# Kernel tuning notes

Hardware: AMD Instinct MI355X
Metric: run time of the kernel (lower is better)

## Reference

```python
import jax, jax.numpy as jnp
import numpy as np

H = 256      # hidden_size
NH = 4       # num_heads
HD = H // NH # head_dim
N_NODES = 2048
N_EDGES = 8192
EPS = 1e-5


def _layer_norm(x, g, b):
    mu = jnp.mean(x, axis=-1, keepdims=True)
    var = jnp.mean((x - mu) ** 2, axis=-1, keepdims=True)
    return (x - mu) * jax.lax.rsqrt(var + EPS) * g + b


def setup_inputs() -> dict:
    key = jax.random.key(0)
    ks = jax.random.split(key, 16)
    s = 1.0 / np.sqrt(H)
    inp = {
        "node_features": jax.random.normal(ks[0], (N_NODES, H), jnp.float32),
        "edge_features": jax.random.normal(ks[1], (N_EDGES, H), jnp.float32),
        "in_proj_w": jax.random.uniform(ks[2], (3 * H, H), jnp.float32, -s, s),
        "in_proj_b": jnp.zeros((3 * H,), jnp.float32),
        "out_proj_w": jax.random.uniform(ks[3], (H, H), jnp.float32, -s, s),
        "out_proj_b": jnp.zeros((H,), jnp.float32),
        "mlp_w1": jax.random.uniform(ks[4], (H, H), jnp.float32, -s, s),
        "mlp_b1": jnp.zeros((H,), jnp.float32),
        "mlp_w2": jax.random.uniform(ks[5], (H, H), jnp.float32, -s, s),
        "mlp_b2": jnp.zeros((H,), jnp.float32),
        "nu_w": jax.random.uniform(ks[6], (H, H), jnp.float32, -s, s),
        "nu_b": jnp.zeros((H,), jnp.float32),
        "ln1_g": jnp.ones((H,), jnp.float32),
        "ln1_b": jnp.zeros((H,), jnp.float32),
        "ln2_g": jnp.ones((H,), jnp.float32),
        "ln2_b": jnp.zeros((H,), jnp.float32),
        "edge_index": jax.random.randint(ks[7], (2, N_EDGES), 0, N_NODES, jnp.int32),
    }
    return inp


def reference(node_features, edge_features, in_proj_w, in_proj_b, out_proj_w, out_proj_b,
              mlp_w1, mlp_b1, mlp_w2, mlp_b2, nu_w, nu_b,
              ln1_g, ln1_b, ln2_g, ln2_b, edge_index):
    x = edge_features  # [E, H]; torch MHA with batch=1, seq=E
    qkv = x @ in_proj_w.T + in_proj_b            # [E, 3H]
    q, k, v = jnp.split(qkv, 3, axis=-1)
    q = q.reshape(N_EDGES, NH, HD)
    k = k.reshape(N_EDGES, NH, HD)
    v = v.reshape(N_EDGES, NH, HD)
    scores = jnp.einsum('qhd,khd->hqk', q, k) / np.sqrt(HD)  # [NH, E, E]
    attn = jax.nn.softmax(scores, axis=-1)
    ctx = jnp.einsum('hqk,khd->qhd', attn, v).reshape(N_EDGES, H)
    attended = ctx @ out_proj_w.T + out_proj_b

    e = _layer_norm(edge_features + attended, ln1_g, ln1_b)
    mlp = jax.nn.relu(e @ mlp_w1.T + mlp_b1) @ mlp_w2.T + mlp_b2
    e = _layer_norm(e + mlp, ln2_g, ln2_b)

    dst = edge_index[1]
    seg_sum = jax.ops.segment_sum(e, dst, num_segments=N_NODES)           # [N, H]
    cnt = jax.ops.segment_sum(jnp.ones((N_EDGES,), e.dtype), dst, num_segments=N_NODES)
    node_updates = seg_sum / jnp.maximum(cnt, 1.0)[:, None]               # scatter_mean
    n = node_features + jax.nn.relu(node_updates @ nu_w.T + nu_b)
    return (n, e)
```

## Files before the change

kernel.cpp:

```cpp
#include <hip/hip_runtime.h>

typedef __bf16 bf16_t;
typedef __bf16 bf16x8 __attribute__((ext_vector_type(8)));
typedef __bf16 bf16x4 __attribute__((ext_vector_type(4)));
typedef unsigned short u16x8 __attribute__((ext_vector_type(8)));
typedef unsigned int u32x4 __attribute__((ext_vector_type(4)));
typedef float f32x4 __attribute__((ext_vector_type(4)));
typedef float f32x16 __attribute__((ext_vector_type(16)));
typedef int i32x2 __attribute__((ext_vector_type(2)));

#define NE 8192
#define NN 2048
#define HH 256
#define NSPLIT 8
#define QSCALE 0.18033688011112042f

#if __has_builtin(__builtin_amdgcn_exp2f)
#define EXP2(x) __builtin_amdgcn_exp2f(x)
#else
#define EXP2(x) exp2f(x)
#endif

__device__ inline f32x4 mfma16(bf16x8 a, bf16x8 b, f32x4 c) {
    return __builtin_amdgcn_mfma_f32_16x16x32_bf16(a, b, c, 0, 0, 0);
}
__device__ inline f32x16 mfma32(bf16x8 a, bf16x8 b, f32x16 c) {
    return __builtin_amdgcn_mfma_f32_32x32x16_bf16(a, b, c, 0, 0, 0);
}
__device__ inline unsigned cvtpk(float lo, float hi) {
    unsigned r;
    asm("v_cvt_pk_bf16_f32 %0, %1, %2" : "=v"(r) : "v"(lo), "v"(hi));
    return r;
}
__device__ inline bf16x8 cvt8(float4 a, float4 b) {
    bf16x8 o;
    o[0] = (bf16_t)a.x; o[1] = (bf16_t)a.y; o[2] = (bf16_t)a.z; o[3] = (bf16_t)a.w;
    o[4] = (bf16_t)b.x; o[5] = (bf16_t)b.y; o[6] = (bf16_t)b.z; o[7] = (bf16_t)b.w;
    return o;
}
__device__ inline bf16x4 cvt4(float4 v) {
    bf16x4 o;
    o[0] = (bf16_t)v.x; o[1] = (bf16_t)v.y; o[2] = (bf16_t)v.z; o[3] = (bf16_t)v.w;
    return o;
}

__global__ __launch_bounds__(256)
void convert_kernel(const float* __restrict__ ef, const float* __restrict__ wq,
                    const float* __restrict__ wo, const float* __restrict__ w1,
                    const float* __restrict__ w2, const float* __restrict__ wn,
                    bf16_t* __restrict__ ebf, bf16_t* __restrict__ bwq,
                    bf16_t* __restrict__ bwo, bf16_t* __restrict__ bw1,
                    bf16_t* __restrict__ bw2, bf16_t* __restrict__ bwn) {
    int i = blockIdx.x * 256 + threadIdx.x;
    ((bf16x4*)ebf)[i] = cvt4(((const float4*)ef)[i]);
    if (i < 49152) ((bf16x4*)bwq)[i] = cvt4(((const float4*)wq)[i]);
    if (i < 16384) {
        ((bf16x4*)bwo)[i] = cvt4(((const float4*)wo)[i]);
        ((bf16x4*)bw1)[i] = cvt4(((const float4*)w1)[i]);
        ((bf16x4*)bw2)[i] = cvt4(((const float4*)w2)[i]);
        ((bf16x4*)bwn)[i] = cvt4(((const float4*)wn)[i]);
    }
}

template<int ACT, int OUTKIND, int QSC, int ADIV>
__global__ __launch_bounds__(256)
void gemm_kernel(const void* __restrict__ Av, const bf16_t* __restrict__ B,
                 const float* __restrict__ bias, void* __restrict__ out,
                 const float* __restrict__ resid, const float* __restrict__ cntp,
                 int M, int N, int K) {
    __shared__ bf16_t As[64][72];
    __shared__ bf16_t Bs[64][72];
    int tid = threadIdx.x;
    int w = tid >> 6, l = tid & 63, hi = l >> 4, c15 = l & 15;
    int wr = w >> 1, wc = w & 1;
    int brow = blockIdx.x * 64, bcol = blockIdx.y * 64;
    int r = tid >> 2, s = tid & 3;

    f32x4 acc[2][2] = {};

    for (int k0 = 0; k0 < K; k0 += 64) {
        __syncthreads();
        if (ADIV) {
            const float* Af = (const float*)Av;
            const float* p = &Af[(long)(brow + r) * K + k0 + s * 16];
            float4 f0 = *(const float4*)p,       f1 = *(const float4*)(p + 4);
            float4 f2 = *(const float4*)(p + 8), f3 = *(const float4*)(p + 12);
            float rc = 1.0f / fmaxf(cntp[brow + r], 1.0f);
            f0.x *= rc; f0.y *= rc; f0.z *= rc; f0.w *= rc;
            f1.x *= rc; f1.y *= rc; f1.z *= rc; f1.w *= rc;
            f2.x *= rc; f2.y *= rc; f2.z *= rc; f2.w *= rc;
            f3.x *= rc; f3.y *= rc; f3.z *= rc; f3.w *= rc;
            *(bf16x8*)&As[r][s * 16]     = cvt8(f0, f1);
            *(bf16x8*)&As[r][s * 16 + 8] = cvt8(f2, f3);
        } else {
            const bf16_t* Ab = (const bf16_t*)Av;
            *(bf16x8*)&As[r][s * 16]     = *(const bf16x8*)&Ab[(long)(brow + r) * K + k0 + s * 16];
            *(bf16x8*)&As[r][s * 16 + 8] = *(const bf16x8*)&Ab[(long)(brow + r) * K + k0 + s * 16 + 8];
        }
        *(bf16x8*)&Bs[r][s * 16]     = *(const bf16x8*)&B[(long)(bcol + r) * K + k0 + s * 16];
        *(bf16x8*)&Bs[r][s * 16 + 8] = *(const bf16x8*)&B[(long)(bcol + r) * K + k0 + s * 16 + 8];
        __syncthreads();
#pragma unroll
        for (int c = 0; c < 2; ++c) {
            bf16x8 af0 = *(const bf16x8*)&As[wr * 32 + c15][c * 32 + hi * 8];
            bf16x8 af1 = *(const bf16x8*)&As[wr * 32 + 16 + c15][c * 32 + hi * 8];
            bf16x8 bf0 = *(const bf16x8*)&Bs[wc * 32 + c15][c * 32 + hi * 8];
            bf16x8 bf1 = *(const bf16x8*)&Bs[wc * 32 + 16 + c15][c * 32 + hi * 8];
            acc[0][0] = mfma16(af0, bf0, acc[0][0]);
            acc[0][1] = mfma16(af0, bf1, acc[0][1]);
            acc[1][0] = mfma16(af1, bf0, acc[1][0]);
            acc[1][1] = mfma16(af1, bf1, acc[1][1]);
        }
    }

    float sc = (QSC && bcol < 256) ? QSCALE : 1.0f;
#pragma unroll
    for (int i = 0; i < 2; ++i)
#pragma unroll
        for (int j = 0; j < 2; ++j)
#pragma unroll
            for (int rg = 0; rg < 4; ++rg) {
                int row = brow + wr * 32 + i * 16 + hi * 4 + rg;
                int col = bcol + wc * 32 + j * 16 + c15;
                float v = (acc[i][j][rg] + bias[col]) * sc;
                if (ACT) v = fmaxf(v, 0.0f);
                if (OUTKIND == 0) {
                    ((float*)out)[(long)row * N + col] = v;
                } else if (OUTKIND == 1) {
                    ((bf16_t*)out)[(long)row * N + col] = (bf16_t)v;
                } else {
                    ((float*)out)[(long)row * N + col] =
                        resid[(long)row * N + col] + fmaxf(v, 0.0f);
                }
            }
}

__global__ __launch_bounds__(256, 2)
void attn_kernel(const bf16_t* __restrict__ qkv, bf16_t* __restrict__ Opart,
                 float* __restrict__ lpart) {
    __shared__ char smem[36864];
    bf16_t (*Ks)[64][72] = (bf16_t (*)[64][72])smem;
    bf16_t (*Vt)[64][72] = (bf16_t (*)[64][72])(smem + 18432);

    int h = blockIdx.x & 3, qb = blockIdx.x >> 2, sp = blockIdx.y;
    int q0 = qb * 256;
    int tid = threadIdx.x;
    int wv = tid >> 6, l = tid & 63, l31 = l & 31, h8 = l >> 5;

    bf16x8 qf[2][4];
#pragma unroll
    for (int qt = 0; qt < 2; ++qt)
#pragma unroll
        for (int dc = 0; dc < 4; ++dc)
            qf[qt][dc] = *(const bf16x8*)&qkv[
                (size_t)(q0 + wv * 64 + qt * 32 + l31) * 768 + h * 64 + dc * 16 + h8 * 8];

    f32x16 o[2][2];
#pragma unroll
    for (int a = 0; a < 2; ++a)
#pragma unroll
        for (int b = 0; b < 2; ++b)
#pragma unroll
            for (int r = 0; r < 16; ++r) o[a][b][r] = 0.f;
    float ls[2] = {0.f, 0.f};

    int kr = tid >> 2, ksc = tid & 3;
    int vp = tid & 31, vc = tid >> 5;
    int kv0 = sp * (NE / NSPLIT);
    const int NT = (NE / NSPLIT) / 64;

    bf16x8 kst0, kst1, vst0, vst1;
    {
        const bf16_t* ksrc = &qkv[(size_t)(kv0 + kr) * 768 + 256 + h * 64 + ksc * 16];
        kst0 = *(const bf16x8*)ksrc; kst1 = *(const bf16x8*)(ksrc + 8);
        const bf16_t* vsrc = &qkv[(size_t)(kv0 + 2 * vp) * 768 + 512 + h * 64 + vc * 8];
        vst0 = *(const bf16x8*)vsrc; vst1 = *(const bf16x8*)(vsrc + 768);
    }
    {
        *(bf16x8*)&Ks[0][kr][ksc * 16]     = kst0;
        *(bf16x8*)&Ks[0][kr][ksc * 16 + 8] = kst1;
        u16x8 ua = __builtin_bit_cast(u16x8, vst0), ub = __builtin_bit_cast(u16x8, vst1);
#pragma unroll
        for (int j = 0; j < 8; ++j) {
            unsigned wd = (unsigned)ua[j] | ((unsigned)ub[j] << 16);
            *(unsigned*)&Vt[0][vc * 8 + j][2 * vp] = wd;
        }
    }

    for (int t = 0; t < NT; ++t) {
        int cur = t & 1;
        __syncthreads();
        if (t + 1 < NT) {
            int kt = kv0 + (t + 1) * 64;
            const bf16_t* ksrc = &qkv[(size_t)(kt + kr) * 768 + 256 + h * 64 + ksc * 16];
            kst0 = *(const bf16x8*)ksrc; kst1 = *(const bf16x8*)(ksrc + 8);
            const bf16_t* vsrc = &qkv[(size_t)(kt + 2 * vp) * 768 + 512 + h * 64 + vc * 8];
            vst0 = *(const bf16x8*)vsrc; vst1 = *(const bf16x8*)(vsrc + 768);
        }

#pragma unroll
        for (int kvt = 0; kvt < 2; ++kvt) {
            bf16x8 kf[4];
#pragma unroll
            for (int dc = 0; dc < 4; ++dc)
                kf[dc] = *(const bf16x8*)&Ks[cur][kvt * 32 + l31][dc * 16 + h8 * 8];
            f32x16 s[2];
#pragma unroll
            for (int qt = 0; qt < 2; ++qt) {
#pragma unroll
                for (int r = 0; r < 16; ++r) s[qt][r] = 0.f;
#pragma unroll
                for (int dc = 0; dc < 4; ++dc)
                    s[qt] = mfma32(kf[dc], qf[qt][dc], s[qt]);
            }
            bf16x8 bfr[2][2];
#pragma unroll
            for (int qt = 0; qt < 2; ++qt) {
                float p[16];
#pragma unroll
                for (int r = 0; r < 16; ++r) { p[r] = EXP2(s[qt][r]); ls[qt] += p[r]; }
#pragma unroll
                for (int half = 0; half < 2; ++half) {
                    i32x2 r0 = __builtin_amdgcn_permlane32_swap(
                        (int)cvtpk(p[8 * half + 0], p[8 * half + 1]),
                        (int)cvtpk(p[8 * half + 4], p[8 * half + 5]), false, false);
                    i32x2 r1 = __builtin_amdgcn_permlane32_swap(
                        (int)cvtpk(p[8 * half + 2], p[8 * half + 3]),
                        (int)cvtpk(p[8 * half + 6], p[8 * half + 7]), false, false);
                    u32x4 wds;
                    wds[0] = (unsigned)r0[0]; wds[1] = (unsigned)r1[0];
                    wds[2] = (unsigned)r0[1]; wds[3] = (unsigned)r1[1];
                    bfr[qt][half] = __builtin_bit_cast(bf16x8, wds);
                }
            }
#pragma unroll
            for (int dt = 0; dt < 2; ++dt) {
                bf16x8 vf[2];
#pragma unroll
                for (int half = 0; half < 2; ++half)
                    vf[half] = *(const bf16x8*)&Vt[cur][dt * 32 + l31][(kvt * 2 + half) * 16 + h8 * 8];
#pragma unroll
                for (int qt = 0; qt < 2; ++qt)
#pragma unroll
                    for (int half = 0; half < 2; ++half)
                        o[dt][qt] = mfma32(vf[half], bfr[qt][half], o[dt][qt]);
            }
        }

        if (t + 1 < NT) {
            int nb = (t + 1) & 1;
            *(bf16x8*)&Ks[nb][kr][ksc * 16]     = kst0;
            *(bf16x8*)&Ks[nb][kr][ksc * 16 + 8] = kst1;
            u16x8 ua = __builtin_bit_cast(u16x8, vst0), ub = __builtin_bit_cast(u16x8, vst1);
#pragma unroll
            for (int j = 0; j < 8; ++j) {
                unsigned wd = (unsigned)ua[j] | ((unsigned)ub[j] << 16);
                *(unsigned*)&Vt[nb][vc * 8 + j][2 * vp] = wd;
            }
        }
    }

#pragma unroll
    for (int qt = 0; qt < 2; ++qt) {
        float lt = ls[qt] + __shfl_xor(ls[qt], 32);
        if (l < 32)
            lpart[((size_t)sp * 4 + h) * NE + q0 + wv * 64 + qt * 32 + l31] = lt;
    }

    float* Of = (float*)smem;
#pragma unroll
    for (int pass = 0; pass < 2; ++pass) {
        __syncthreads();
        if ((wv >> 1) == pass) {
#pragma unroll
            for (int dt = 0; dt < 2; ++dt)
#pragma unroll
                for (int qt = 0; qt < 2; ++qt)
#pragma unroll
                    for (int r = 0; r < 16; ++r) {
                        int qrel = (wv & 1) * 64 + qt * 32 + l31;
                        int d = dt * 32 + (r & 3) + 8 * (r >> 2) + 4 * h8;
                        Of[qrel * 68 + d] = o[dt][qt][r];
                    }
        }
        __syncthreads();
        {
            int rr = tid >> 1, hf = tid & 1;
            bf16_t* dst = &Opart[(size_t)sp * NE * 256 +
                                 (size_t)(q0 + pass * 128 + rr) * 256 + h * 64 + hf * 32];
#pragma unroll
            for (int i = 0; i < 4; ++i) {
                float4 va = *(float4*)&Of[rr * 68 + hf * 32 + i * 8];
                float4 vb = *(float4*)&Of[rr * 68 + hf * 32 + i * 8 + 4];
                bf16x8 ob;
                ob[0] = (bf16_t)va.x; ob[1] = (bf16_t)va.y;
                ob[2] = (bf16_t)va.z; ob[3] = (bf16_t)va.w;
                ob[4] = (bf16_t)vb.x; ob[5] = (bf16_t)vb.y;
                ob[6] = (bf16_t)vb.z; ob[7] = (bf16_t)vb.w;
                *(bf16x8*)&dst[i * 8] = ob;
            }
        }
    }
}

__global__ __launch_bounds__(256)
void attn_merge_kernel(const bf16_t* __restrict__ Opart, const float* __restrict__ lpart,
                       bf16_t* __restrict__ ctx) {
    int i = blockIdx.x * 256 + threadIdx.x;
    int q = i >> 5;
    int h = (i & 31) >> 3;
    float sum[8] = {};
    float lsum = 0.f;
#pragma unroll
    for (int sp = 0; sp < NSPLIT; ++sp) {
        bf16x8 v = ((const bf16x8*)Opart)[(size_t)sp * (NE * 32) + i];
#pragma unroll
        for (int j = 0; j < 8; ++j) sum[j] += (float)v[j];
        lsum += lpart[((size_t)sp * 4 + h) * NE + q];
    }
    float rl = 1.0f / lsum;
    bf16x8 c;
#pragma unroll
    for (int j = 0; j < 8; ++j) c[j] = (bf16_t)(sum[j] * rl);
    ((bf16x8*)ctx)[i] = c;
}

template<int YBF16, int WRITE_BF16>
__global__ __launch_bounds__(256)
void ln_kernel(const float* __restrict__ x, const void* __restrict__ yv,
               const float* __restrict__ g, const float* __restrict__ b,
               float* __restrict__ outf, bf16_t* __restrict__ outb) {
    int row = blockIdx.x * 4 + (threadIdx.x >> 6);
    int l = threadIdx.x & 63;
    float4 v = ((const float4*)&x[(long)row * 256])[l];
    float y0, y1, y2, y3;
    if (YBF16) {
        bf16x4 t = ((const bf16x4*)yv)[(long)row * 64 + l];
        y0 = (float)t[0]; y1 = (float)t[1]; y2 = (float)t[2]; y3 = (float)t[3];
    } else {
        float4 t = ((const float4*)yv)[(long)row * 64 + l];
        y0 = t.x; y1 = t.y; y2 = t.z; y3 = t.w;
    }
    float a0 = v.x + y0, a1 = v.y + y1, a2 = v.z + y2, a3 = v.w + y3;

    float s = a0 + a1 + a2 + a3;
#pragma unroll
    for (int off = 1; off < 64; off <<= 1) s += __shfl_xor(s, off);
    float mu = s * (1.0f / 256.0f);

    float d0 = a0 - mu, d1 = a1 - mu, d2 = a2 - mu, d3 = a3 - mu;
    float q = d0 * d0 + d1 * d1 + d2 * d2 + d3 * d3;
#pragma unroll
    for (int off = 1; off < 64; off <<= 1) q += __shfl_xor(q, off);
    float rs = rsqrtf(q * (1.0f / 256.0f) + 1e-5f);

    float4 gg = ((const float4*)g)[l];
    float4 bb = ((const float4*)b)[l];
    float o0 = d0 * rs * gg.x + bb.x;
    float o1 = d1 * rs * gg.y + bb.y;
    float o2 = d2 * rs * gg.z + bb.z;
    float o3 = d3 * rs * gg.w + bb.w;
    float4 ov; ov.x = o0; ov.y = o1; ov.z = o2; ov.w = o3;
    ((float4*)&outf[(long)row * 256])[l] = ov;
    if (WRITE_BF16) {
        bf16x4 ob;
        ob[0] = (bf16_t)o0; ob[1] = (bf16_t)o1; ob[2] = (bf16_t)o2; ob[3] = (bf16_t)o3;
        ((bf16x4*)&outb[(long)row * 256])[l] = ob;
    }
}

__global__ __launch_bounds__(256)
void scatter_kernel(const float* __restrict__ e, const int* __restrict__ ei,
                    float* __restrict__ acc, float* __restrict__ cnt) {
    int edge = blockIdx.x;
    int dst = ei[NE + edge];
    int t = threadIdx.x;
    atomicAdd(&acc[(long)dst * 256 + t], e[(long)edge * 256 + t]);
    if (t == 0) atomicAdd(&cnt[dst], 1.0f);
}

extern "C" void kernel_launch(void* const* d_in, const int* in_sizes, int n_in,
                              void* d_out, int out_size, void* d_ws, size_t ws_size,
                              hipStream_t stream) {
    const float* node_features = (const float*)d_in[0];
    const float* edge_features = (const float*)d_in[1];
    const float* in_proj_w  = (const float*)d_in[2];
    const float* in_proj_b  = (const float*)d_in[3];
    const float* out_proj_w = (const float*)d_in[4];
    const float* out_proj_b = (const float*)d_in[5];
    const float* mlp_w1 = (const float*)d_in[6];
    const float* mlp_b1 = (const float*)d_in[7];
    const float* mlp_w2 = (const float*)d_in[8];
    const float* mlp_b2 = (const float*)d_in[9];
    const float* nu_w   = (const float*)d_in[10];
    const float* nu_b   = (const float*)d_in[11];
    const float* ln1_g  = (const float*)d_in[12];
    const float* ln1_b  = (const float*)d_in[13];
    const float* ln2_g  = (const float*)d_in[14];
    const float* ln2_b  = (const float*)d_in[15];
    const int*   edge_index = (const int*)d_in[16];

    char* ws = (char*)d_ws;
    size_t off = 0;
    auto alloc = [&](size_t bytes) {
        char* p = ws + off;
        off = (off + bytes + 255) & ~(size_t)255;
        return p;
    };
    bf16_t* ebf   = (bf16_t*)alloc(NE * HH * 2);
    bf16_t* bwq   = (bf16_t*)alloc(768 * 256 * 2);
    bf16_t* bwo   = (bf16_t*)alloc(256 * 256 * 2);
    bf16_t* bw1   = (bf16_t*)alloc(256 * 256 * 2);
    bf16_t* bw2   = (bf16_t*)alloc(256 * 256 * 2);
    bf16_t* bwn   = (bf16_t*)alloc(256 * 256 * 2);
    bf16_t* qkv   = (bf16_t*)alloc((size_t)NE * 768 * 2);
    bf16_t* ctx   = (bf16_t*)alloc((size_t)NE * HH * 2);
    float*  lpart = (float*)alloc((size_t)NSPLIT * 4 * NE * 4);
    float*  acc   = (float*)alloc((size_t)(NN * HH + NN) * 4);
    float*  cnt   = acc + (size_t)NN * HH;
    size_t offB = off;
    bf16_t* Opart = (bf16_t*)alloc((size_t)NSPLIT * NE * HH * 2);
    off = offB;
    bf16_t* attended = (bf16_t*)alloc((size_t)NE * HH * 2);
    float*  e1f   = (float*)alloc((size_t)NE * HH * 4);
    bf16_t* e1b   = (bf16_t*)alloc((size_t)NE * HH * 2);
    bf16_t* hbuf  = (bf16_t*)alloc((size_t)NE * HH * 2);
    bf16_t* mlpout = (bf16_t*)alloc((size_t)NE * HH * 2);

    float* nout = (float*)d_out;
    float* eout = (float*)d_out + (size_t)NN * HH;

    convert_kernel<<<2048, 256, 0, stream>>>(edge_features, in_proj_w, out_proj_w,
                                             mlp_w1, mlp_w2, nu_w,
                                             ebf, bwq, bwo, bw1, bw2, bwn);

    gemm_kernel<0, 1, 1, 0><<<dim3(NE / 64, 768 / 64), 256, 0, stream>>>(
        ebf, bwq, in_proj_b, qkv, nullptr, nullptr, NE, 768, 256);

    attn_kernel<<<dim3(128, NSPLIT), 256, 0, stream>>>(qkv, Opart, lpart);
    attn_merge_kernel<<<1024, 256, 0, stream>>>(Opart, lpart, ctx);

    gemm_kernel<0, 1, 0, 0><<<dim3(NE / 64, 256 / 64), 256, 0, stream>>>(
        ctx, bwo, out_proj_b, attended, nullptr, nullptr, NE, 256, 256);

    ln_kernel<1, 1><<<NE / 4, 256, 0, stream>>>(edge_features, attended, ln1_g, ln1_b,
                                                e1f, e1b);

    gemm_kernel<1, 1, 0, 0><<<dim3(NE / 64, 256 / 64), 256, 0, stream>>>(
        e1b, bw1, mlp_b1, hbuf, nullptr, nullptr, NE, 256, 256);

    gemm_kernel<0, 1, 0, 0><<<dim3(NE / 64, 256 / 64), 256, 0, stream>>>(
        hbuf, bw2, mlp_b2, mlpout, nullptr, nullptr, NE, 256, 256);

    ln_kernel<1, 0><<<NE / 4, 256, 0, stream>>>(e1f, mlpout, ln2_g, ln2_b,
                                                eout, (bf16_t*)nullptr);

    hipMemsetAsync(acc, 0, (size_t)(NN * HH + NN) * 4, stream);
    scatter_kernel<<<NE, 256, 0, stream>>>(eout, edge_index, acc, cnt);

    gemm_kernel<0, 2, 0, 1><<<dim3(NN / 64, 256 / 64), 256, 0, stream>>>(
        acc, bwn, nu_b, nout, node_features, cnt, NN, 256, 256);
}
```

Before: 147.3 us.

## Fuse scatter into second layernorm, drop fp32 residual, halve attention splits

The scatter-mean atomics move into the second layernorm kernel, which removes a separate launch and a re-read of the edge output. The fp32 copy of the first layernorm output is dropped, and the second layernorm reads the bf16 copy as its residual. That saves a 8MB write and read but lowers residual precision. NSPLIT goes from 8 to 4, which halves the partial-output buffer and the merge traffic at the cost of less attention parallelism.

After: 162.2 us. +10.2%, slower.

```diff
diff --git a/kernel.cpp b/kernel.cpp
--- a/kernel.cpp
+++ b/kernel.cpp
@@ -12,7 +12,7 @@
 #define NE 8192
 #define NN 2048
 #define HH 256
-#define NSPLIT 8
+#define NSPLIT 4
 #define QSCALE 0.18033688011112042f
 
 #if __has_builtin(__builtin_amdgcn_exp2f)
@@ -325,15 +325,23 @@
     ((bf16x8*)ctx)[i] = c;
 }
 
-template<int YBF16, int WRITE_BF16>
+template<int XBF16, int YBF16, int WRITE_F32, int WRITE_BF16, int SCATTER>
 __global__ __launch_bounds__(256)
-void ln_kernel(const float* __restrict__ x, const void* __restrict__ yv,
+void ln_kernel(const void* __restrict__ xv, const void* __restrict__ yv,
                const float* __restrict__ g, const float* __restrict__ b,
-               float* __restrict__ outf, bf16_t* __restrict__ outb) {
+               float* __restrict__ outf, bf16_t* __restrict__ outb,
+               const int* __restrict__ ei, float* __restrict__ acc,
+               float* __restrict__ cnt) {
     int row = blockIdx.x * 4 + (threadIdx.x >> 6);
     int l = threadIdx.x & 63;
-    float4 v = ((const float4*)&x[(long)row * 256])[l];
-    float y0, y1, y2, y3;
+    float x0, x1, x2, x3, y0, y1, y2, y3;
+    if (XBF16) {
+        bf16x4 t = ((const bf16x4*)xv)[(long)row * 64 + l];
+        x0 = (float)t[0]; x1 = (float)t[1]; x2 = (float)t[2]; x3 = (float)t[3];
+    } else {
+        float4 t = ((const float4*)xv)[(long)row * 64 + l];
+        x0 = t.x; x1 = t.y; x2 = t.z; x3 = t.w;
+    }
     if (YBF16) {
         bf16x4 t = ((const bf16x4*)yv)[(long)row * 64 + l];
         y0 = (float)t[0]; y1 = (float)t[1]; y2 = (float)t[2]; y3 = (float)t[3];
@@ -341,7 +349,7 @@
         float4 t = ((const float4*)yv)[(long)row * 64 + l];
         y0 = t.x; y1 = t.y; y2 = t.z; y3 = t.w;
     }
-    float a0 = v.x + y0, a1 = v.y + y1, a2 = v.z + y2, a3 = v.w + y3;
+    float a0 = x0 + y0, a1 = x1 + y1, a2 = x2 + y2, a3 = x3 + y3;
 
     float s = a0 + a1 + a2 + a3;
 #pragma unroll
@@ -360,23 +368,24 @@
     float o1 = d1 * rs * gg.y + bb.y;
     float o2 = d2 * rs * gg.z + bb.z;
     float o3 = d3 * rs * gg.w + bb.w;
-    float4 ov; ov.x = o0; ov.y = o1; ov.z = o2; ov.w = o3;
-    ((float4*)&outf[(long)row * 256])[l] = ov;
+    if (WRITE_F32) {
+        float4 ov; ov.x = o0; ov.y = o1; ov.z = o2; ov.w = o3;
+        ((float4*)&outf[(long)row * 256])[l] = ov;
+    }
     if (WRITE_BF16) {
         bf16x4 ob;
         ob[0] = (bf16_t)o0; ob[1] = (bf16_t)o1; ob[2] = (bf16_t)o2; ob[3] = (bf16_t)o3;
         ((bf16x4*)&outb[(long)row * 256])[l] = ob;
     }
-}
-
-__global__ __launch_bounds__(256)
-void scatter_kernel(const float* __restrict__ e, const int* __restrict__ ei,
-                    float* __restrict__ acc, float* __restrict__ cnt) {
-    int edge = blockIdx.x;
-    int dst = ei[NE + edge];
-    int t = threadIdx.x;
-    atomicAdd(&acc[(long)dst * 256 + t], e[(long)edge * 256 + t]);
-    if (t == 0) atomicAdd(&cnt[dst], 1.0f);
+    if (SCATTER) {
+        int dst = ei[NE + row];
+        float* ap = &acc[(long)dst * 256 + l * 4];
+        atomicAdd(ap + 0, o0);
+        atomicAdd(ap + 1, o1);
+        atomicAdd(ap + 2, o2);
+        atomicAdd(ap + 3, o3);
+        if (l == 0) atomicAdd(&cnt[dst], 1.0f);
+    }
 }
 
 extern "C" void kernel_launch(void* const* d_in, const int* in_sizes, int n_in,
@@ -422,7 +431,6 @@
     bf16_t* Opart = (bf16_t*)alloc((size_t)NSPLIT * NE * HH * 2);
     off = offB;
     bf16_t* attended = (bf16_t*)alloc((size_t)NE * HH * 2);
-    float*  e1f   = (float*)alloc((size_t)NE * HH * 4);
     bf16_t* e1b   = (bf16_t*)alloc((size_t)NE * HH * 2);
     bf16_t* hbuf  = (bf16_t*)alloc((size_t)NE * HH * 2);
     bf16_t* mlpout = (bf16_t*)alloc((size_t)NE * HH * 2);
@@ -434,6 +442,8 @@
                                              mlp_w1, mlp_w2, nu_w,
                                              ebf, bwq, bwo, bw1, bw2, bwn);
 
+    hipMemsetAsync(acc, 0, (size_t)(NN * HH + NN) * 4, stream);
+
     gemm_kernel<0, 1, 1, 0><<<dim3(NE / 64, 768 / 64), 256, 0, stream>>>(
         ebf, bwq, in_proj_b, qkv, nullptr, nullptr, NE, 768, 256);
 
@@ -443,8 +453,9 @@
     gemm_kernel<0, 1, 0, 0><<<dim3(NE / 64, 256 / 64), 256, 0, stream>>>(
         ctx, bwo, out_proj_b, attended, nullptr, nullptr, NE, 256, 256);
 
-    ln_kernel<1, 1><<<NE / 4, 256, 0, stream>>>(edge_features, attended, ln1_g, ln1_b,
-                                                e1f, e1b);
+    ln_kernel<0, 1, 0, 1, 0><<<NE / 4, 256, 0, stream>>>(
+        edge_features, attended, ln1_g, ln1_b, nullptr, e1b,
+        nullptr, nullptr, nullptr);
 
     gemm_kernel<1, 1, 0, 0><<<dim3(NE / 64, 256 / 64), 256, 0, stream>>>(
         e1b, bw1, mlp_b1, hbuf, nullptr, nullptr, NE, 256, 256);
@@ -452,11 +463,9 @@
     gemm_kernel<0, 1, 0, 0><<<dim3(NE / 64, 256 / 64), 256, 0, stream>>>(
         hbuf, bw2, mlp_b2, mlpout, nullptr, nullptr, NE, 256, 256);
 
-    ln_kernel<1, 0><<<NE / 4, 256, 0, stream>>>(e1f, mlpout, ln2_g, ln2_b,
-                                                eout, (bf16_t*)nullptr);
-
-    hipMemsetAsync(acc, 0, (size_t)(NN * HH + NN) * 4, stream);
-    scatter_kernel<<<NE, 256, 0, stream>>>(eout, edge_index, acc, cnt);
+    ln_kernel<1, 1, 1, 0, 1><<<NE / 4, 256, 0, stream>>>(
+        e1b, mlpout, ln2_g, ln2_b, eout, nullptr,
+        edge_index, acc, cnt);
 
     gemm_kernel<0, 2, 0, 1><<<dim3(NN / 64, 256 / 64), 256, 0, stream>>>(
         acc, bwn, nu_b, nout, node_features, cnt, NN, 256, 256);
```
